# Optimization experiments

Hardware: AMD Instinct MI355X
Metric: run time of the kernel (lower is better)

Reference implementation:

```python
import jax, jax.numpy as jnp
import numpy as np

B, IN_DIM, HID, T, OUT_DIM = 2048, 1024, 1024, 32, 512


def setup_inputs() -> dict:
    key = jax.random.key(0)
    ks = jax.random.split(key, 10)
    s_in = 1.0 / np.sqrt(IN_DIM)
    s_h = 1.0 / np.sqrt(HID)
    return {
        "x": jax.random.normal(ks[0], (B, IN_DIM), dtype=jnp.float32),
        "W_in": jax.random.uniform(ks[1], (HID, IN_DIM), jnp.float32, -s_in, s_in),
        "b_in": jax.random.uniform(ks[2], (HID,), jnp.float32, -s_in, s_in),
        "W_ih": jax.random.uniform(ks[3], (4 * HID, HID), jnp.float32, -s_h, s_h),
        "b_ih": jax.random.uniform(ks[4], (4 * HID,), jnp.float32, -s_h, s_h),
        "W_hh": jax.random.uniform(ks[5], (4 * HID, HID), jnp.float32, -s_h, s_h),
        "b_hh": jax.random.uniform(ks[6], (4 * HID,), jnp.float32, -s_h, s_h),
        "W_out": jax.random.uniform(ks[7], (OUT_DIM, HID), jnp.float32, -s_h, s_h),
        "b_out": jax.random.uniform(ks[8], (OUT_DIM,), jnp.float32, -s_h, s_h),
    }


def reference(x, W_in, b_in, W_ih, b_ih, W_hh, b_hh, W_out, b_out):
    # lstm_in + relu (dropout = identity in eval mode)
    h0 = jax.nn.relu(x @ W_in.T + b_in)          # [B, H]
    c0 = jnp.zeros_like(h0)

    def step(carry, _):
        h, c = carry
        # seq is None: the cell input at each step is the previous hidden state
        gates = h @ W_ih.T + b_ih + h @ W_hh.T + b_hh   # [B, 4H]
        i, f, g, o = jnp.split(gates, 4, axis=-1)        # torch chunk order i,f,g,o
        i = jax.nn.sigmoid(i)
        f = jax.nn.sigmoid(f)
        g = jnp.tanh(g)
        o = jax.nn.sigmoid(o)
        c_new = f * c + i * g
        h_new = o * jnp.tanh(c_new)
        return (h_new, c_new), h_new

    (_, _), hs = jax.lax.scan(step, (h0, c0), xs=None, length=T)  # hs: [T, B, H]
    hs = jnp.transpose(hs, (1, 0, 2))                              # [B, T, H]
    return hs @ W_out.T + b_out                                    # [B, T, OUT]
```

## Files before the change

kernel.cpp:

```cpp
#include <hip/hip_runtime.h>
#include <hip/hip_bf16.h>
#include <cstdint>
#include <cstddef>

#define BATCH   2048
#define HIDDIM  1024
#define TSTEPS  32
#define OUTDIM  512
#define KDIM    1024
#define HS_SLOTS 9

using bf16 = __hip_bfloat16;
typedef __bf16 bf16x8 __attribute__((ext_vector_type(8)));
typedef float  f32x4  __attribute__((ext_vector_type(4)));

__device__ __forceinline__ void async_load16(const void* g, void* l) {
    __builtin_amdgcn_global_load_lds(
        (__attribute__((address_space(1))) unsigned int*)(g),
        (__attribute__((address_space(3))) unsigned int*)(l),
        16, 0, 0);
}

__device__ __forceinline__ float sigf(float x) {
    return 1.f / (1.f + __expf(-x));
}
__device__ __forceinline__ float tanh_stable(float x) {
    const float a = __builtin_fabsf(x);
    const float e = __expf(2.f * a);
    const float r = 1.f - 2.f / (e + 1.f);
    return __builtin_copysignf(r, x);
}

__launch_bounds__(512, 2)
__global__ void lstm_step(const bf16* __restrict__ h_in, const bf16* __restrict__ Wc,
                          const float* __restrict__ bc,
                          float* __restrict__ cstate, bf16* __restrict__ h_out,
                          bf16* __restrict__ hs, int t, int slot,
                          const bf16* __restrict__ Wo, const float* __restrict__ b_out,
                          float* __restrict__ out, int t0, int gates_blocks) {
    __shared__ __align__(16) char smem[49152];
    bf16* lA = (bf16*)smem;
    bf16* lB = (bf16*)(smem + 16384);

    const int tid  = threadIdx.x;
    const int wid  = tid >> 6;
    const int lane = tid & 63;
    const int wr   = wid >> 2;
    const int wc   = wid & 3;
    const int lrow = lane & 15;
    const int lkg  = lane >> 4;

    const int bid   = blockIdx.x;
    const bool is_out = (bid >= gates_blocks);

    int m0, n0;
    const bf16* Abase;
    const bf16* Bbase;
    const float* bias;
    if (!is_out) {
        n0 = (bid & 15) * 256;
        m0 = (bid >> 4) * 128;
        Abase = h_in; Bbase = Wc; bias = bc;
    } else {
        const int ob = bid - gates_blocks;
        n0 = (ob & 1) * 256;
        m0 = (ob >> 1) * 128;
        Abase = hs; Bbase = Wo; bias = b_out;
    }

    float bs[4];
#pragma unroll
    for (int ni = 0; ni < 4; ++ni) bs[ni] = bias[n0 + wc * 64 + ni * 16 + lrow];

    const int r0 = tid >> 2;
    const int c0 = (tid & 3) * 8;
    int arow;
    if (!is_out) {
        arow = m0 + r0;
    } else {
        const int rr = m0 + r0;
        arow = (rr >> 3) * HS_SLOTS + (t0 + (rr & 7)) % HS_SLOTS;
    }
    const bf16* gA  = Abase + (size_t)arow * KDIM + c0;
    const bf16* gB0 = Bbase + (size_t)(n0 + r0) * KDIM + c0;
    const bf16* gB1 = Bbase + (size_t)(n0 + 128 + r0) * KDIM + c0;

    f32x4 acc[4][4];
#pragma unroll
    for (int i = 0; i < 4; ++i)
#pragma unroll
        for (int j = 0; j < 4; ++j) acc[i][j] = (f32x4){0.f, 0.f, 0.f, 0.f};

    auto STAGE = [&](int buf, int ko) {
        bf16* a_d = lA + buf * 4096 + wid * 512;
        bf16* b_d0 = lB + buf * 8192 + wid * 512;
        bf16* b_d1 = lB + buf * 8192 + 4096 + wid * 512;
        async_load16(gA + ko, a_d);
        async_load16(gB0 + ko, b_d0);
        async_load16(gB1 + ko, b_d1);
    };

    STAGE(0, 0);
    __syncthreads();
    int cur = 0;
    for (int kt = 0; kt < KDIM / 32; ++kt) {
        if (kt < KDIM / 32 - 1) STAGE(cur ^ 1, (kt + 1) * 32);
        const bf16* bufA = lA + cur * 4096;
        const bf16* bufB = lB + cur * 8192;
        bf16x8 af[4], bfr[4];
#pragma unroll
        for (int mi = 0; mi < 4; ++mi)
            af[mi] = *(const bf16x8*)&bufA[(wr * 64 + mi * 16 + lrow) * 32 + lkg * 8];
#pragma unroll
        for (int ni = 0; ni < 4; ++ni)
            bfr[ni] = *(const bf16x8*)&bufB[(wc * 64 + ni * 16 + lrow) * 32 + lkg * 8];
#pragma unroll
        for (int mi = 0; mi < 4; ++mi)
#pragma unroll
            for (int ni = 0; ni < 4; ++ni)
                acc[mi][ni] = __builtin_amdgcn_mfma_f32_16x16x32_bf16(
                    af[mi], bfr[ni], acc[mi][ni], 0, 0, 0);
        __syncthreads();
        cur ^= 1;
    }

    if (!is_out) {
        float* cbuf = (float*)smem;
        const int lrd = tid >> 4;
        const int j4  = (tid & 15) * 4;
        const int jg0 = n0 >> 2;
#pragma unroll
        for (int p = 0; p < 4; ++p) {
            if (wr == (p >> 1)) {
#pragma unroll
                for (int mm = 0; mm < 2; ++mm) {
                    const int mi = ((p & 1) << 1) | mm;
#pragma unroll
                    for (int ni = 0; ni < 4; ++ni) {
                        const int lc = wc * 64 + ni * 16 + lrow;
#pragma unroll
                        for (int r = 0; r < 4; ++r) {
                            const int lpr = mm * 16 + lkg * 4 + r;
                            cbuf[lpr * 260 + lc] = acc[mi][ni][r] + bs[ni];
                        }
                    }
                }
            }
            __syncthreads();
            const int grow = m0 + p * 32 + lrd;
            const float* rowp = cbuf + lrd * 260;
#pragma unroll
            for (int q = 0; q < 4; ++q) {
                const f32x4 v = *(const f32x4*)&rowp[(j4 + q) * 4];
                const float gi = sigf(v[0]);
                const float gf = sigf(v[1]);
                const float gg = tanh_stable(v[2]);
                const float go = sigf(v[3]);
                const int j = jg0 + j4 + q;
                const size_t off = (size_t)grow * 1024 + j;
                const float cold = (t == 0) ? 0.f : cstate[off];
                const float cn = gf * cold + gi * gg;
                const float hn = go * tanh_stable(cn);
                cstate[off] = cn;
                const bf16 hb = __float2bfloat16(hn);
                h_out[off] = hb;
                hs[((size_t)grow * HS_SLOTS + slot) * 1024 + j] = hb;
            }
            __syncthreads();
        }
    } else {
#pragma unroll
        for (int mi = 0; mi < 4; ++mi) {
#pragma unroll
            for (int ni = 0; ni < 4; ++ni) {
                const f32x4 v = acc[mi][ni];
                const int c = n0 + wc * 64 + ni * 16 + lrow;
                const int rb = m0 + wr * 64 + mi * 16 + lkg * 4;
#pragma unroll
                for (int r = 0; r < 4; ++r) {
                    const int row = rb + r;
                    const int orow = (row >> 3) * TSTEPS + t0 + (row & 7);
                    out[(size_t)orow * OUTDIM + c] = v[r] + bs[ni];
                }
            }
        }
    }
}

__launch_bounds__(256, 2)
__global__ void gemm_h0(const bf16* __restrict__ A, const bf16* __restrict__ Bm,
                        const float* __restrict__ bias, bf16* __restrict__ C) {
    __shared__ __align__(16) bf16 lA[128 * 32];
    __shared__ __align__(16) bf16 lB[128 * 32];

    const int tid  = threadIdx.x;
    const int wid  = tid >> 6;
    const int lane = tid & 63;
    const int m0   = blockIdx.y * 128;
    const int n0   = blockIdx.x * 128;
    const int wr   = wid >> 1;
    const int wc   = wid & 1;
    const int lrow = lane & 15;
    const int lkg  = lane >> 4;

    f32x4 acc[4][4];
#pragma unroll
    for (int i = 0; i < 4; ++i)
#pragma unroll
        for (int j = 0; j < 4; ++j) acc[i][j] = (f32x4){0.f, 0.f, 0.f, 0.f};

    const int r0 = tid >> 2;
    const int c0 = (tid & 3) * 8;
    const bf16* gA0 = A  + (size_t)(m0 + r0) * KDIM + c0;
    const bf16* gA1 = A  + (size_t)(m0 + 64 + r0) * KDIM + c0;
    const bf16* gB0 = Bm + (size_t)(n0 + r0) * KDIM + c0;
    const bf16* gB1 = Bm + (size_t)(n0 + 64 + r0) * KDIM + c0;
    bf16* lAq0 = &lA[(size_t)(wid * 64) * 8];
    bf16* lAq1 = &lA[(size_t)(256 + wid * 64) * 8];
    bf16* lBq0 = &lB[(size_t)(wid * 64) * 8];
    bf16* lBq1 = &lB[(size_t)(256 + wid * 64) * 8];

    for (int kt = 0; kt < KDIM / 32; ++kt) {
        const int ko = kt * 32;
        async_load16(gA0 + ko, lAq0);
        async_load16(gA1 + ko, lAq1);
        async_load16(gB0 + ko, lBq0);
        async_load16(gB1 + ko, lBq1);
        __syncthreads();
        bf16x8 af[4], bfr[4];
#pragma unroll
        for (int mi = 0; mi < 4; ++mi)
            af[mi] = *(const bf16x8*)&lA[(size_t)(wr * 64 + mi * 16 + lrow) * 32 + lkg * 8];
#pragma unroll
        for (int ni = 0; ni < 4; ++ni)
            bfr[ni] = *(const bf16x8*)&lB[(size_t)(wc * 64 + ni * 16 + lrow) * 32 + lkg * 8];
#pragma unroll
        for (int mi = 0; mi < 4; ++mi)
#pragma unroll
            for (int ni = 0; ni < 4; ++ni)
                acc[mi][ni] = __builtin_amdgcn_mfma_f32_16x16x32_bf16(
                    af[mi], bfr[ni], acc[mi][ni], 0, 0, 0);
        __syncthreads();
    }
#pragma unroll
    for (int mi = 0; mi < 4; ++mi) {
#pragma unroll
        for (int ni = 0; ni < 4; ++ni) {
            const f32x4 v = acc[mi][ni];
            const int c = n0 + wc * 64 + ni * 16 + lrow;
            const int rb = m0 + wr * 64 + mi * 16 + lkg * 4;
            const float bsv = bias[c];
#pragma unroll
            for (int r = 0; r < 4; ++r) {
                const float val = v[r] + bsv;
                C[(size_t)(rb + r) * 1024 + c] = __float2bfloat16(val > 0.f ? val : 0.f);
            }
        }
    }
}

__global__ void prep_wc(const float* __restrict__ Wih, const float* __restrict__ Whh,
                        const float* __restrict__ bih, const float* __restrict__ bhh,
                        bf16* __restrict__ Wc, float* __restrict__ bc) {
    const int base = (blockIdx.x * 256 + threadIdx.x) * 4;
    const int r = base >> 10;
    const int k = base & 1023;
    const int pr = (r & 1023) * 4 + (r >> 10);
    const float4 a = *(const float4*)(Wih + base);
    const float4 b = *(const float4*)(Whh + base);
    bf16* d = Wc + (size_t)pr * 1024 + k;
    d[0] = __float2bfloat16(a.x + b.x);
    d[1] = __float2bfloat16(a.y + b.y);
    d[2] = __float2bfloat16(a.z + b.z);
    d[3] = __float2bfloat16(a.w + b.w);
    if (base < 4096) {
#pragma unroll
        for (int s = 0; s < 4; ++s) {
            const int e = base + s;
            bc[(e & 1023) * 4 + (e >> 10)] = bih[e] + bhh[e];
        }
    }
}

__global__ void f2b(const float* __restrict__ s, bf16* __restrict__ d, int n) {
    const int i = (blockIdx.x * 256 + threadIdx.x) * 4;
    if (i < n) {
        const float4 v = *(const float4*)(s + i);
        d[i + 0] = __float2bfloat16(v.x);
        d[i + 1] = __float2bfloat16(v.y);
        d[i + 2] = __float2bfloat16(v.z);
        d[i + 3] = __float2bfloat16(v.w);
    }
}

extern "C" void kernel_launch(void* const* d_in, const int* in_sizes, int n_in,
                              void* d_out, int out_size, void* d_ws, size_t ws_size,
                              hipStream_t stream) {
    const float* x     = (const float*)d_in[0];
    const float* W_in  = (const float*)d_in[1];
    const float* b_in  = (const float*)d_in[2];
    const float* W_ih  = (const float*)d_in[3];
    const float* b_ih  = (const float*)d_in[4];
    const float* W_hh  = (const float*)d_in[5];
    const float* b_hh  = (const float*)d_in[6];
    const float* W_out = (const float*)d_in[7];
    const float* b_out = (const float*)d_in[8];
    float* out = (float*)d_out;

    char* ws = (char*)d_ws;
    bf16* Wc   = (bf16*)ws;  ws += (size_t)4096 * 1024 * 2;
    bf16* Wi_b = (bf16*)ws;  ws += (size_t)1024 * 1024 * 2;
    bf16* Wo_b = (bf16*)ws;  ws += (size_t)512  * 1024 * 2;
    bf16* x_b  = (bf16*)ws;  ws += (size_t)2048 * 1024 * 2;
    bf16* hb0  = (bf16*)ws;  ws += (size_t)2048 * 1024 * 2;
    bf16* hb1  = (bf16*)ws;  ws += (size_t)2048 * 1024 * 2;
    bf16* hs   = (bf16*)ws;  ws += (size_t)2048 * HS_SLOTS * 1024 * 2;
    float* bc  = (float*)ws; ws += (size_t)4096 * 4;
    float* cst = (float*)ws; ws += (size_t)2048 * 1024 * 4;

    prep_wc<<<4096 * 1024 / (256 * 4), 256, 0, stream>>>(W_ih, W_hh, b_ih, b_hh, Wc, bc);
    f2b<<<2048 * 1024 / (256 * 4), 256, 0, stream>>>(x, x_b, 2048 * 1024);
    f2b<<<1024 * 1024 / (256 * 4), 256, 0, stream>>>(W_in, Wi_b, 1024 * 1024);
    f2b<<<512 * 1024 / (256 * 4), 256, 0, stream>>>(W_out, Wo_b, 512 * 1024);

    {
        dim3 g(HIDDIM / 128, BATCH / 128);
        gemm_h0<<<g, 256, 0, stream>>>(x_b, Wi_b, b_in, hb0);
    }

    for (int t = 0; t < TSTEPS; ++t) {
        bf16* h_in  = (t & 1) ? hb1 : hb0;
        bf16* h_out = (t & 1) ? hb0 : hb1;
        const bool fuse = (t == 8 || t == 16 || t == 24);
        const int blocks = fuse ? 512 : 256;
        lstm_step<<<blocks, 512, 0, stream>>>(h_in, Wc, bc, cst, h_out, hs,
                                              t, t % HS_SLOTS,
                                              Wo_b, b_out, out, t - 8, 256);
    }
    lstm_step<<<256, 512, 0, stream>>>(hb0, Wc, bc, cst, hb1, hs,
                                       0, 0, Wo_b, b_out, out, 24, 0);
    (void)in_sizes; (void)n_in; (void)out_size; (void)ws_size;
}
```

Baseline: 1.326 ms.

## Triple-buffer GEMM main loop with explicit vmcnt waits and MFMA priority

Replaces the double-buffered K loop with a three-stage ring of LDS buffers, prefetching two tiles ahead. Explicit s_waitcnt vmcnt counts replace the blanket __syncthreads, so each iteration waits only for the tile it is about to use. The MFMA block is wrapped in s_setprio and scheduling barriers. The bias load moves after the loop so it does not disturb the vmcnt accounting. LDS use grows to 72KB per block, which constrains occupancy at two blocks per CU.

Measured after the change: 1.200 ms. -9.5%, faster.

```diff
diff --git a/kernel.cpp b/kernel.cpp
--- a/kernel.cpp
+++ b/kernel.cpp
@@ -30,6 +30,33 @@
     const float r = 1.f - 2.f / (e + 1.f);
     return __builtin_copysignf(r, x);
 }
+
+#define MAINLOOP_ITER(VMNT)                                                    \
+    asm volatile("s_waitcnt vmcnt(" VMNT ")" ::: "memory");                    \
+    __builtin_amdgcn_s_barrier();                                              \
+    __builtin_amdgcn_sched_barrier(0);                                         \
+    {                                                                          \
+        const bf16* bufA_ = lA + cur * 4096;                                   \
+        const bf16* bufB_ = lB + cur * 8192;                                   \
+        bf16x8 af[4], bfr[4];                                                  \
+        _Pragma("unroll")                                                      \
+        for (int mi = 0; mi < 4; ++mi)                                         \
+            af[mi] = *(const bf16x8*)&bufA_[(wr * 64 + mi * 16 + lrow) * 32 + lkg * 8];  \
+        _Pragma("unroll")                                                      \
+        for (int ni = 0; ni < 4; ++ni)                                         \
+            bfr[ni] = *(const bf16x8*)&bufB_[(wc * 64 + ni * 16 + lrow) * 32 + lkg * 8]; \
+        __builtin_amdgcn_s_setprio(1);                                         \
+        _Pragma("unroll")                                                      \
+        for (int mi = 0; mi < 4; ++mi) {                                       \
+            _Pragma("unroll")                                                  \
+            for (int ni = 0; ni < 4; ++ni)                                     \
+                acc[mi][ni] = __builtin_amdgcn_mfma_f32_16x16x32_bf16(         \
+                    af[mi], bfr[ni], acc[mi][ni], 0, 0, 0);                    \
+        }                                                                      \
+        __builtin_amdgcn_s_setprio(0);                                         \
+    }                                                                          \
+    __builtin_amdgcn_sched_barrier(0);                                         \
+    __builtin_amdgcn_s_barrier();
 
 __launch_bounds__(512, 2)
 __global__ void lstm_step(const bf16* __restrict__ h_in, const bf16* __restrict__ Wc,
@@ -38,9 +65,9 @@
                           bf16* __restrict__ hs, int t, int slot,
                           const bf16* __restrict__ Wo, const float* __restrict__ b_out,
                           float* __restrict__ out, int t0, int gates_blocks) {
-    __shared__ __align__(16) char smem[49152];
+    __shared__ __align__(16) char smem[73728];
     bf16* lA = (bf16*)smem;
-    bf16* lB = (bf16*)(smem + 16384);
+    bf16* lB = (bf16*)(smem + 24576);
 
     const int tid  = threadIdx.x;
     const int wid  = tid >> 6;
@@ -68,10 +95,6 @@
         Abase = hs; Bbase = Wo; bias = b_out;
     }
 
-    float bs[4];
-#pragma unroll
-    for (int ni = 0; ni < 4; ++ni) bs[ni] = bias[n0 + wc * 64 + ni * 16 + lrow];
-
     const int r0 = tid >> 2;
     const int c0 = (tid & 3) * 8;
     int arow;
@@ -92,7 +115,7 @@
         for (int j = 0; j < 4; ++j) acc[i][j] = (f32x4){0.f, 0.f, 0.f, 0.f};
 
     auto STAGE = [&](int buf, int ko) {
-        bf16* a_d = lA + buf * 4096 + wid * 512;
+        bf16* a_d  = lA + buf * 4096 + wid * 512;
         bf16* b_d0 = lB + buf * 8192 + wid * 512;
         bf16* b_d1 = lB + buf * 8192 + 4096 + wid * 512;
         async_load16(gA + ko, a_d);
@@ -101,28 +124,22 @@
     };
 
     STAGE(0, 0);
-    __syncthreads();
+    STAGE(1, 32);
+    STAGE(2, 64);
     int cur = 0;
-    for (int kt = 0; kt < KDIM / 32; ++kt) {
-        if (kt < KDIM / 32 - 1) STAGE(cur ^ 1, (kt + 1) * 32);
-        const bf16* bufA = lA + cur * 4096;
-        const bf16* bufB = lB + cur * 8192;
-        bf16x8 af[4], bfr[4];
-#pragma unroll
-        for (int mi = 0; mi < 4; ++mi)
-            af[mi] = *(const bf16x8*)&bufA[(wr * 64 + mi * 16 + lrow) * 32 + lkg * 8];
-#pragma unroll
-        for (int ni = 0; ni < 4; ++ni)
-            bfr[ni] = *(const bf16x8*)&bufB[(wc * 64 + ni * 16 + lrow) * 32 + lkg * 8];
-#pragma unroll
-        for (int mi = 0; mi < 4; ++mi)
-#pragma unroll
-            for (int ni = 0; ni < 4; ++ni)
-                acc[mi][ni] = __builtin_amdgcn_mfma_f32_16x16x32_bf16(
-                    af[mi], bfr[ni], acc[mi][ni], 0, 0, 0);
-        __syncthreads();
-        cur ^= 1;
-    }
+    for (int kt = 0; kt < 30; ++kt) {
+        MAINLOOP_ITER("6")
+        if (kt < 29) STAGE(cur, (kt + 3) * 32);
+        cur = (cur == 2) ? 0 : cur + 1;
+    }
+    MAINLOOP_ITER("3")
+    cur = (cur == 2) ? 0 : cur + 1;
+    MAINLOOP_ITER("0")
+    __builtin_amdgcn_sched_barrier(0);
+
+    float bs[4];
+#pragma unroll
+    for (int ni = 0; ni < 4; ++ni) bs[ni] = bias[n0 + wc * 64 + ni * 16 + lrow];
 
     if (!is_out) {
         float* cbuf = (float*)smem;
```
